# Kernel optimization log

Hardware: AMD Instinct MI355X
Metric: run time of the kernel (lower is better)

## Reference

```python
import jax, jax.numpy as jnp
import numpy as np

N_NODES = 50000
N_EDGES = 800000
IN_C, HID_C, OUT_C = 512, 256, 2


def gcn_conv(x, W, b, src, dst, norm, num_nodes):
    # x: [N, Fin]; W: [Fin, Fout]; src/dst/norm: [E+N] (self-loops included)
    h = x @ W                                   # [N, Fout]
    msgs = h[src] * norm[:, None]               # gather + scale, [E+N, Fout]
    out = jax.ops.segment_sum(msgs, dst, num_segments=num_nodes)  # scatter-add
    return out + b


def _gcn_norm(src, dst, num_nodes):
    # PyG gcn_norm with add_self_loops=True, unit edge weights
    loop = jnp.arange(num_nodes, dtype=src.dtype)
    src2 = jnp.concatenate([src, loop])
    dst2 = jnp.concatenate([dst, loop])
    w = jnp.ones(src2.shape[0], dtype=jnp.float32)
    deg = jax.ops.segment_sum(w, dst2, num_segments=num_nodes)
    dinv = jnp.where(deg > 0, jax.lax.rsqrt(deg), 0.0)
    norm = dinv[src2] * dinv[dst2]
    return src2, dst2, norm


def setup_inputs() -> dict:
    key = jax.random.key(0)
    ks = jax.random.split(key, 4)
    x = jax.random.normal(ks[0], (N_NODES, IN_C), dtype=jnp.float32)
    edge_index = jax.random.randint(ks[1], (2, N_EDGES), 0, N_NODES, dtype=jnp.int64)
    W1 = jax.random.normal(ks[2], (IN_C, HID_C), dtype=jnp.float32) / np.sqrt(IN_C)
    b1 = jnp.zeros((HID_C,), dtype=jnp.float32)
    W2 = jax.random.normal(ks[3], (HID_C, OUT_C), dtype=jnp.float32) / np.sqrt(HID_C)
    b2 = jnp.zeros((OUT_C,), dtype=jnp.float32)
    return {"x": x, "edge_index": edge_index, "W1": W1, "b1": b1, "W2": W2, "b2": b2}


def reference(x, edge_index, W1, b1, W2, b2):
    n = x.shape[0]
    src, dst, norm = _gcn_norm(edge_index[0], edge_index[1], n)
    h = gcn_conv(x, W1, b1, src, dst, norm, n)
    h = jax.nn.relu(h)
    # dropout is identity in eval mode (training=False)
    out = gcn_conv(h, W2, b2, src, dst, norm, n)
    return out
```

## Files before the change

kernel.cpp:

```cpp
#include <hip/hip_runtime.h>
#include <hip/hip_bf16.h>
#include <stdint.h>

#define N_NODES 50000
#define N_EDGES 800000
#define IN_C 512
#define HID_C 256
#define CAP 96

typedef __attribute__((ext_vector_type(8))) short bf16x8;
typedef __attribute__((ext_vector_type(4))) float f32x4;
typedef __attribute__((address_space(3))) uint32_t lds_u32_t;
typedef __attribute__((address_space(1))) const uint32_t g_u32_t;

__device__ __forceinline__ void g2l16(const void* g, void* l) {
    __builtin_amdgcn_global_load_lds((g_u32_t*)g, (lds_u32_t*)l, 16, 0, 0);
}

__device__ __forceinline__ unsigned short f2bf(float f) {
    uint32_t u = __float_as_uint(f);
    uint32_t r = (u + 0x7fff + ((u >> 16) & 1)) >> 16;
    return (unsigned short)r;
}


#define ZERO_BLOCKS ((N_NODES + 255) / 256)
#define PREP_BLOCKS (ZERO_BLOCKS + 256)

__global__ __launch_bounds__(256) void prep_kernel(int* __restrict__ cursor,
                                                   const float* __restrict__ W1,
                                                   unsigned short* __restrict__ Wt) {
    const int t = threadIdx.x;
    if (blockIdx.x < ZERO_BLOCKS) {
        const int i = blockIdx.x * 256 + t;
        if (i < N_NODES) cursor[i] = 0;
    } else {
        const int c = blockIdx.x - ZERO_BLOCKS;
        for (int k = t; k < IN_C; k += 256)
            Wt[c * IN_C + k] = f2bf(W1[k * HID_C + c]);
    }
}


#define FILL_BLOCKS ((N_EDGES + 1023) / 1024)
#define GEMM_BLOCKS ((N_NODES + 127) / 128)
#define GF_BLOCKS (FILL_BLOCKS + GEMM_BLOCKS)
#define NKT 16

__global__ __launch_bounds__(512) void gf_kernel(
    const float* __restrict__ A,
    const unsigned short* __restrict__ Bt,
    unsigned short* __restrict__ hB,
    int M,
    const int* __restrict__ src,
    const int* __restrict__ dst,
    int* cursor,
    unsigned short* __restrict__ bucket)
{
    __shared__ float          Asf[2][128 * 32];
    __shared__ unsigned short Bs[2][256 * 32];
    const int t = threadIdx.x;

    if (blockIdx.x < FILL_BLOCKS) {
        const int i0 = (blockIdx.x * 512 + t) * 2;
        if (i0 >= N_EDGES) return;
        int s0, d0, s1 = -1, d1 = -1;
        if (i0 + 2 <= N_EDGES) {
            const int2 s2 = *(const int2*)&src[i0];
            const int2 d2 = *(const int2*)&dst[i0];
            s0 = s2.x; s1 = s2.y; d0 = d2.x; d1 = d2.y;
        } else {
            s0 = src[i0]; d0 = dst[i0];
        }
        const int p0 = atomicAdd(&cursor[d0], 1);
        if (p0 < CAP) bucket[d0 * CAP + p0] = (unsigned short)s0;
        if (s1 >= 0) {
            const int p1 = atomicAdd(&cursor[d1], 1);
            if (p1 < CAP) bucket[d1 * CAP + p1] = (unsigned short)s1;
        }
        return;
    }

    const int m0 = (blockIdx.x - FILL_BLOCKS) * 128;
    const int w = t >> 6, l = t & 63;
    const int wr = (w >> 2) * 64;
    const int wc = (w & 3) * 64;
    const int l15 = l & 15, l4 = l >> 4;

    f32x4 acc[4][4] = {};

    auto stage = [&](int buf, int kt) {
        #pragma unroll
        for (int q = 0; q < 2; ++q) {
            const int idx = q * 512 + t;
            const int row = idx >> 3;
            const int ck  = (idx & 7) ^ (row & 7);
            int gr = m0 + row; if (gr >= M) gr = M - 1;
            g2l16(&A[(size_t)gr * IN_C + kt * 32 + ck * 4], &Asf[buf][idx * 4]);
        }
        #pragma unroll
        for (int q = 0; q < 2; ++q) {
            const int idx = q * 512 + t;
            const int row = idx >> 2;
            const int ck  = (idx & 3) ^ (row & 3) ^ ((row >> 2) & 3);
            g2l16(&Bt[(size_t)row * IN_C + kt * 32 + ck * 8], &Bs[buf][idx * 8]);
        }
    };
    auto compute = [&](int buf) {
        bf16x8 a[4], b[4];
        #pragma unroll
        for (int mi = 0; mi < 4; ++mi) {
            const int r  = wr + mi * 16 + l15;
            const int s0 = l4 * 2;
            const float4 lo = *(const float4*)&Asf[buf][r * 32 + ((s0    ) ^ (r & 7)) * 4];
            const float4 hi = *(const float4*)&Asf[buf][r * 32 + ((s0 + 1) ^ (r & 7)) * 4];
            union { bf16x8 v; __hip_bfloat162 h2[4]; } cv;
            cv.h2[0] = __float22bfloat162_rn(make_float2(lo.x, lo.y));
            cv.h2[1] = __float22bfloat162_rn(make_float2(lo.z, lo.w));
            cv.h2[2] = __float22bfloat162_rn(make_float2(hi.x, hi.y));
            cv.h2[3] = __float22bfloat162_rn(make_float2(hi.z, hi.w));
            a[mi] = cv.v;
        }
        #pragma unroll
        for (int nj = 0; nj < 4; ++nj) {
            const int r  = wc + nj * 16 + l15;
            const int ck = l4 ^ (r & 3) ^ ((r >> 2) & 3);
            b[nj] = *(const bf16x8*)&Bs[buf][r * 32 + ck * 8];
        }
        #pragma unroll
        for (int mi = 0; mi < 4; ++mi)
            #pragma unroll
            for (int nj = 0; nj < 4; ++nj)
                acc[mi][nj] = __builtin_amdgcn_mfma_f32_16x16x32_bf16(
                    a[mi], b[nj], acc[mi][nj], 0, 0, 0);
    };

    stage(0, 0);
    asm volatile("s_waitcnt vmcnt(0)" ::: "memory");
    __builtin_amdgcn_s_barrier();
    int cur = 0;
    for (int kt = 0; kt < NKT; ++kt) {
        if (kt < NKT - 1) {
            stage(cur ^ 1, kt + 1);
            asm volatile("s_waitcnt vmcnt(4)" ::: "memory");
        } else {
            asm volatile("s_waitcnt vmcnt(0)" ::: "memory");
        }
        __builtin_amdgcn_s_barrier();
        compute(cur);
        __builtin_amdgcn_s_barrier();
        cur ^= 1;
    }

    #pragma unroll
    for (int mi = 0; mi < 4; ++mi)
        #pragma unroll
        for (int nj = 0; nj < 4; ++nj)
            #pragma unroll
            for (int rr = 0; rr < 4; ++rr) {
                const int m = m0 + wr + mi * 16 + l4 * 4 + rr;
                const int n = wc + nj * 16 + l15;
                if (m < M) hB[(size_t)m * HID_C + n] = f2bf(acc[mi][nj][rr]);
            }
}


__device__ __forceinline__ void fma8(float* acc, uint4 r, float w) {
    acc[0] += __uint_as_float((r.x & 0xffffu) << 16) * w;
    acc[1] += __uint_as_float(r.x & 0xffff0000u) * w;
    acc[2] += __uint_as_float((r.y & 0xffffu) << 16) * w;
    acc[3] += __uint_as_float(r.y & 0xffff0000u) * w;
    acc[4] += __uint_as_float((r.z & 0xffffu) << 16) * w;
    acc[5] += __uint_as_float(r.z & 0xffff0000u) * w;
    acc[6] += __uint_as_float((r.w & 0xffffu) << 16) * w;
    acc[7] += __uint_as_float(r.w & 0xffff0000u) * w;
}

__global__ __launch_bounds__(256) void agg1_kernel(const unsigned short* __restrict__ h,
                                                   const int* __restrict__ cursor,
                                                   const unsigned short* __restrict__ bucket,
                                                   const float* __restrict__ b1,
                                                   const float* __restrict__ W2,
                                                   float* __restrict__ h2) {
    const int node = blockIdx.x * 8 + (threadIdx.x >> 5);
    const int g = threadIdx.x & 31;
    const int f0 = g << 3;
    int cnt = cursor[node]; if (cnt > CAP) cnt = CAP;
    const float dv_d = rsqrtf((float)(cursor[node] + 1));

    float acc[8] = {};
    {
        const uint4 rs = *(const uint4*)&h[(size_t)node * HID_C + f0];
        fma8(acc, rs, dv_d);
    }

    const unsigned short* bkt = &bucket[node * CAP];
    for (int base = 0; base < cnt; base += 32) {
        const int rem = cnt - base;
        const int c32 = rem < 32 ? rem : 32;
        int idx = 0; float dv_s = 0.f;
        if (g < c32) {
            idx  = bkt[base + g];
            dv_s = rsqrtf((float)(cursor[idx] + 1));
        }
        int i = 0;
        for (; i + 4 <= c32; i += 4) {
            const int   i0 = __shfl(idx, i,     32); const float w0 = __shfl(dv_s, i,     32);
            const int   i1 = __shfl(idx, i + 1, 32); const float w1 = __shfl(dv_s, i + 1, 32);
            const int   i2 = __shfl(idx, i + 2, 32); const float w2 = __shfl(dv_s, i + 2, 32);
            const int   i3 = __shfl(idx, i + 3, 32); const float w3 = __shfl(dv_s, i + 3, 32);
            const uint4 r0 = *(const uint4*)&h[(size_t)i0 * HID_C + f0];
            const uint4 r1 = *(const uint4*)&h[(size_t)i1 * HID_C + f0];
            const uint4 r2 = *(const uint4*)&h[(size_t)i2 * HID_C + f0];
            const uint4 r3 = *(const uint4*)&h[(size_t)i3 * HID_C + f0];
            fma8(acc, r0, w0); fma8(acc, r1, w1); fma8(acc, r2, w2); fma8(acc, r3, w3);
        }
        for (; i < c32; ++i) {
            const int   ii = __shfl(idx, i, 32);
            const float w  = __shfl(dv_s, i, 32);
            const uint4 r  = *(const uint4*)&h[(size_t)ii * HID_C + f0];
            fma8(acc, r, w);
        }
    }

    const float4 ba = *(const float4*)&b1[f0];
    const float4 bb = *(const float4*)&b1[f0 + 4];
    float v[8];
    v[0] = fmaxf(acc[0] * dv_d + ba.x, 0.f); v[1] = fmaxf(acc[1] * dv_d + ba.y, 0.f);
    v[2] = fmaxf(acc[2] * dv_d + ba.z, 0.f); v[3] = fmaxf(acc[3] * dv_d + ba.w, 0.f);
    v[4] = fmaxf(acc[4] * dv_d + bb.x, 0.f); v[5] = fmaxf(acc[5] * dv_d + bb.y, 0.f);
    v[6] = fmaxf(acc[6] * dv_d + bb.z, 0.f); v[7] = fmaxf(acc[7] * dv_d + bb.w, 0.f);

    float c0 = 0.f, c1 = 0.f;
    #pragma unroll
    for (int q = 0; q < 4; ++q) {
        const float4 wv = *(const float4*)&W2[f0 * 2 + q * 4];
        c0 += v[2*q] * wv.x + v[2*q+1] * wv.z;
        c1 += v[2*q] * wv.y + v[2*q+1] * wv.w;
    }
    #pragma unroll
    for (int o = 16; o > 0; o >>= 1) {
        c0 += __shfl_down(c0, o, 32);
        c1 += __shfl_down(c1, o, 32);
    }
    if (g == 0) *(float2*)&h2[node * 2] = make_float2(c0, c1);
}


__global__ void agg2_kernel(const float* __restrict__ h2,
                            const int* __restrict__ cursor,
                            const unsigned short* __restrict__ bucket,
                            const float* __restrict__ b2,
                            float* __restrict__ out, int n_nodes) {
    const int n = blockIdx.x * blockDim.x + threadIdx.x;
    if (n >= n_nodes) return;
    int cnt = cursor[n]; if (cnt > CAP) cnt = CAP;
    const float dv_d = rsqrtf((float)(cursor[n] + 1));
    const float2 ps = *(const float2*)&h2[n * 2];
    float a0 = dv_d * ps.x, a1 = dv_d * ps.y;
    const unsigned short* bkt = &bucket[n * CAP];
    int i = 0;
    for (; i + 4 <= cnt; i += 4) {
        const uint2 q4 = *(const uint2*)&bkt[i];
        const int s0 = q4.x & 0xffff, s1 = q4.x >> 16;
        const int s2 = q4.y & 0xffff, s3 = q4.y >> 16;
        const float w0 = rsqrtf((float)(cursor[s0] + 1));
        const float w1 = rsqrtf((float)(cursor[s1] + 1));
        const float w2 = rsqrtf((float)(cursor[s2] + 1));
        const float w3 = rsqrtf((float)(cursor[s3] + 1));
        const float2 p0 = *(const float2*)&h2[s0 * 2];
        const float2 p1 = *(const float2*)&h2[s1 * 2];
        const float2 p2 = *(const float2*)&h2[s2 * 2];
        const float2 p3 = *(const float2*)&h2[s3 * 2];
        a0 += p0.x * w0 + p1.x * w1 + p2.x * w2 + p3.x * w3;
        a1 += p0.y * w0 + p1.y * w1 + p2.y * w2 + p3.y * w3;
    }
    for (; i < cnt; ++i) {
        const int s = bkt[i];
        const float w = rsqrtf((float)(cursor[s] + 1));
        const float2 p = *(const float2*)&h2[s * 2];
        a0 += p.x * w;
        a1 += p.y * w;
    }
    out[n * 2 + 0] = b2[0] + dv_d * a0;
    out[n * 2 + 1] = b2[1] + dv_d * a1;
}


static inline size_t align_up(size_t x) { return (x + 255) & ~(size_t)255; }

extern "C" void kernel_launch(void* const* d_in, const int* in_sizes, int n_in,
                              void* d_out, int out_size, void* d_ws, size_t ws_size,
                              hipStream_t stream) {
    const float* x   = (const float*)d_in[0];
    const int*   ei  = (const int*)d_in[1];
    const float* W1  = (const float*)d_in[2];
    const float* b1  = (const float*)d_in[3];
    const float* W2  = (const float*)d_in[4];
    const float* b2  = (const float*)d_in[5];
    float* out = (float*)d_out;

    const int* e_src = ei;
    const int* e_dst = ei + N_EDGES;

    char* ws = (char*)d_ws;
    int*   cursor   = (int*)ws;             ws += align_up((size_t)N_NODES * 4);
    unsigned short* bucket = (unsigned short*)ws; ws += align_up((size_t)N_NODES * CAP * 2);
    unsigned short* Wt = (unsigned short*)ws; ws += align_up((size_t)HID_C * IN_C * 2);
    unsigned short* h  = (unsigned short*)ws; ws += align_up((size_t)N_NODES * HID_C * 2);
    float* h2       = (float*)ws;           ws += align_up((size_t)N_NODES * 2 * 4);

    const int nb_n = (N_NODES + 255) / 256;

    prep_kernel<<<PREP_BLOCKS, 256, 0, stream>>>(cursor, W1, Wt);
    gf_kernel<<<GF_BLOCKS, 512, 0, stream>>>(x, Wt, h, N_NODES,
                                             e_src, e_dst, cursor, bucket);
    agg1_kernel<<<N_NODES / 8, 256, 0, stream>>>(h, cursor, bucket, b1, W2, h2);
    agg2_kernel<<<nb_n, 256, 0, stream>>>(h2, cursor, bucket, b2, out, N_NODES);
}
```

Baseline: 143.8 us.

## Partition edge bucket fill by destination residue and launch GEMM blocks first

The fill phase now splits each 8192-edge chunk across 8 blocks, each handling only destinations whose low 3 bits match its partition. This is meant to spread atomic and bucket writes so each block touches a subset of nodes, and to place GEMM blocks first in the grid so they are scheduled early. The cost is that every fill block reads all edges of its chunk, which multiplies edge index reads by eight. The unsigned short bucket storage is unchanged.

```diff
diff --git a/kernel.cpp b/kernel.cpp
--- a/kernel.cpp
+++ b/kernel.cpp
@@ -42,9 +42,10 @@
 }
 
 
-#define FILL_BLOCKS ((N_EDGES + 1023) / 1024)
 #define GEMM_BLOCKS ((N_NODES + 127) / 128)
-#define GF_BLOCKS (FILL_BLOCKS + GEMM_BLOCKS)
+#define CHUNKS ((N_EDGES + 8191) / 8192)
+#define FILL_BLOCKS (CHUNKS * 8)
+#define GF_BLOCKS (GEMM_BLOCKS + FILL_BLOCKS)
 #define NKT 16
 
 __global__ __launch_bounds__(512) void gf_kernel(
@@ -61,27 +62,37 @@
     __shared__ unsigned short Bs[2][256 * 32];
     const int t = threadIdx.x;
 
-    if (blockIdx.x < FILL_BLOCKS) {
-        const int i0 = (blockIdx.x * 512 + t) * 2;
-        if (i0 >= N_EDGES) return;
-        int s0, d0, s1 = -1, d1 = -1;
-        if (i0 + 2 <= N_EDGES) {
-            const int2 s2 = *(const int2*)&src[i0];
-            const int2 d2 = *(const int2*)&dst[i0];
-            s0 = s2.x; s1 = s2.y; d0 = d2.x; d1 = d2.y;
-        } else {
-            s0 = src[i0]; d0 = dst[i0];
-        }
-        const int p0 = atomicAdd(&cursor[d0], 1);
-        if (p0 < CAP) bucket[d0 * CAP + p0] = (unsigned short)s0;
-        if (s1 >= 0) {
-            const int p1 = atomicAdd(&cursor[d1], 1);
-            if (p1 < CAP) bucket[d1 * CAP + p1] = (unsigned short)s1;
+    if (blockIdx.x >= GEMM_BLOCKS) {
+        const int fb = blockIdx.x - GEMM_BLOCKS;
+        const int p  = fb & 7;
+        const int base = (fb >> 3) * 8192 + t * 16;
+        #pragma unroll
+        for (int j = 0; j < 4; ++j) {
+            const int i = base + j * 4;
+            if (i >= N_EDGES) break;
+            const int4 d4 = *(const int4*)&dst[i];
+            const int4 s4 = *(const int4*)&src[i];
+            if ((d4.x & 7) == p) {
+                const int q = atomicAdd(&cursor[d4.x], 1);
+                if (q < CAP) bucket[d4.x * CAP + q] = (unsigned short)s4.x;
+            }
+            if ((d4.y & 7) == p) {
+                const int q = atomicAdd(&cursor[d4.y], 1);
+                if (q < CAP) bucket[d4.y * CAP + q] = (unsigned short)s4.y;
+            }
+            if ((d4.z & 7) == p) {
+                const int q = atomicAdd(&cursor[d4.z], 1);
+                if (q < CAP) bucket[d4.z * CAP + q] = (unsigned short)s4.z;
+            }
+            if ((d4.w & 7) == p) {
+                const int q = atomicAdd(&cursor[d4.w], 1);
+                if (q < CAP) bucket[d4.w * CAP + q] = (unsigned short)s4.w;
+            }
         }
         return;
     }
 
-    const int m0 = (blockIdx.x - FILL_BLOCKS) * 128;
+    const int m0 = blockIdx.x * 128;
     const int w = t >> 6, l = t & 63;
     const int wr = (w >> 2) * 64;
     const int wc = (w & 3) * 64;
```

Result: faster. 139.2 us (-3.2%).
